# Kernel optimization log

Hardware: AMD Instinct MI355X
Metric: run time of the kernel (lower is better)

The kernel has to match this reference:

```python
import jax, jax.numpy as jnp
import numpy as np

NUM_USERS = 100000
NUM_ITEMS = 200000
EMB_DIM = 64
NUM_LAYERS = 3
NUM_INTER = 1000000
BATCH = 16384


def setup_inputs() -> dict:
    key = jax.random.key(0)
    k1, k2, k3, k4, k5, k6, k7 = jax.random.split(key, 7)
    # xavier-uniform-ish init for embeddings
    bound_u = float(np.sqrt(6.0 / (NUM_USERS + EMB_DIM)))
    bound_i = float(np.sqrt(6.0 / (NUM_ITEMS + EMB_DIM)))
    user_emb = jax.random.uniform(k1, (NUM_USERS, EMB_DIM), jnp.float32, -bound_u, bound_u)
    item_emb = jax.random.uniform(k2, (NUM_ITEMS, EMB_DIM), jnp.float32, -bound_i, bound_i)
    layer_weights = jax.random.uniform(k3, (NUM_LAYERS + 1,), jnp.float32)
    inter_users = jax.random.randint(k4, (NUM_INTER,), 0, NUM_USERS, jnp.int32)
    inter_items = jax.random.randint(k5, (NUM_INTER,), 0, NUM_ITEMS, jnp.int32)
    user_ids = jax.random.randint(k6, (BATCH,), 0, NUM_USERS, jnp.int32)
    item_ids = jax.random.randint(k7, (BATCH,), 0, NUM_ITEMS, jnp.int32)
    return {
        "user_emb": user_emb,
        "item_emb": item_emb,
        "layer_weights": layer_weights,
        "inter_users": inter_users,
        "inter_items": inter_items,
        "user_ids": user_ids,
        "item_ids": item_ids,
    }


def reference(user_emb, item_emb, layer_weights, inter_users, inter_items, user_ids, item_ids):
    n_users = user_emb.shape[0]
    n_items = item_emb.shape[0]
    n_nodes = n_users + n_items

    # Symmetrized bipartite edge list: (u -> i+n_users) and (i+n_users -> u)
    rows = inter_users
    cols = inter_items + n_users
    src = jnp.concatenate([rows, cols])  # [2E]
    dst = jnp.concatenate([cols, rows])  # [2E]

    # Symmetric degree normalization: D^{-1/2} A D^{-1/2}
    deg = jax.ops.segment_sum(jnp.ones_like(src, dtype=jnp.float32), src,
                              num_segments=n_nodes)
    dinv = jnp.where(deg > 0, jax.lax.rsqrt(jnp.maximum(deg, 1.0)) * (deg > 0), 0.0)
    dinv = jnp.where(deg > 0, deg ** -0.5, 0.0)
    edge_w = dinv[src] * dinv[dst]  # [2E]

    emb = jnp.concatenate([user_emb, item_emb], axis=0)  # [N, D]
    weights = jax.nn.softmax(layer_weights)

    final = weights[0] * emb
    for layer in range(NUM_LAYERS):
        # SpMM: out[src] += w * emb[dst]
        emb = jax.ops.segment_sum(edge_w[:, None] * emb[dst], src,
                                  num_segments=n_nodes)
        final = final + weights[layer + 1] * emb

    u_final = final[:n_users]
    i_final = final[n_users:]

    user_vectors = u_final[user_ids]   # [B, D]
    item_vectors = i_final[item_ids]   # [B, D]
    scores = jnp.sum(user_vectors * item_vectors, axis=1)  # [B]
    return scores
```

## Files before the change

### kernel.cpp

```cpp
#include <hip/hip_runtime.h>
#include <math.h>

#define NUM_USERS 100000
#define NUM_ITEMS 200000
#define N_NODES   300000
#define EMB       64
#define NUM_INTER 1000000
#define BATCH     16384

#define BSHIFT 9
#define BNODES 512
#define NBKT   ((N_NODES + BNODES - 1) / BNODES)
#define CAP    6144
#define RSHIFT 13
#define RSLOTS (1 << RSHIFT)
#define EDGES_PER_BLOCK 4096
#define AB_BLOCKS ((NUM_INTER + EDGES_PER_BLOCK - 1) / EDGES_PER_BLOCK)
#define QMARK_BLOCKS ((BATCH * 2) / 256)

#define PROP_BLOCKS ((N_NODES * 8 + 255) / 256)

typedef int      vint4 __attribute__((ext_vector_type(4)));
typedef _Float16 half8 __attribute__((ext_vector_type(8)));

#define PMASK 0x7FFFFu

__global__ __launch_bounds__(256) void bucket_scatter_k(
        const int* __restrict__ iu, const int* __restrict__ ii,
        const int* __restrict__ uid, const int* __restrict__ iid,
        int* __restrict__ cursor , unsigned* __restrict__ pairs,
        unsigned char* __restrict__ qflag, unsigned char* __restrict__ flag,
        const float* __restrict__ lw, float* __restrict__ w4,
        _Float16* __restrict__ semb, _Float16* __restrict__ z1, _Float16* __restrict__ z2) {
    int tid = threadIdx.x;
    if (blockIdx.x < QMARK_BLOCKS) {
        int t = blockIdx.x * 256 + tid;
        int node = (t & 1) ? (NUM_USERS + iid[t >> 1]) : uid[t >> 1];
        qflag[node] = 1;
        flag[node]  = 1;
        return;
    }
    if (blockIdx.x == QMARK_BLOCKS) {
        if (tid < 96) {
            unsigned* p = (tid < 32) ? (unsigned*)semb : (tid < 64) ? (unsigned*)z1 : (unsigned*)z2;
            p[(size_t)N_NODES * 32 + (tid & 31)] = 0u;
        }
        if (tid == 0) {
            float a = lw[0], b = lw[1], c = lw[2], d = lw[3];
            float m = fmaxf(fmaxf(a, b), fmaxf(c, d));
            float e0 = expf(a - m), e1 = expf(b - m), e2 = expf(c - m), e3 = expf(d - m);
            float sm = e0 + e1 + e2 + e3;
            w4[0] = e0 / sm; w4[1] = e1 / sm; w4[2] = e2 / sm; w4[3] = e3 / sm;
        }
        return;
    }
    __shared__ int hist[NBKT];
    __shared__ int gbase[NBKT];
    int bid = blockIdx.x - QMARK_BLOCKS - 1;
    for (int b = tid; b < NBKT; b += 256) hist[b] = 0;
    __syncthreads();

    int e0 = bid * EDGES_PER_BLOCK;
    int u[16], it[16];
    unsigned pk[32];
    #pragma unroll
    for (int k = 0; k < 16; ++k) {
        int e = e0 + k * 256 + tid;
        bool v = (e < NUM_INTER);
        u[k]  = v ? iu[e] : -1;
        it[k] = v ? (NUM_USERS + ii[e]) : -1;
    }
    #pragma unroll
    for (int k = 0; k < 16; ++k) {
        if (u[k] >= 0) {
            int b0 = u[k] >> BSHIFT;
            int r0 = atomicAdd(&hist[b0], 1);
            pk[2 * k] = ((unsigned)b0 << 13) | (unsigned)r0;
            int b1 = it[k] >> BSHIFT;
            int r1 = atomicAdd(&hist[b1], 1);
            pk[2 * k + 1] = ((unsigned)b1 << 13) | (unsigned)r1;
        }
    }
    __syncthreads();
    for (int b = tid; b < NBKT; b += 256) {
        int c = hist[b];
        if (c) gbase[b] = atomicAdd(&cursor[b * 16], c);
    }
    __syncthreads();
    #pragma unroll
    for (int k = 0; k < 16; ++k) {
        if (u[k] >= 0) {
            unsigned p0 = pk[2 * k];
            int b0 = (int)(p0 >> 13);
            int s0 = gbase[b0] + (int)(p0 & 0x1fffu);
            if (s0 < CAP)
                pairs[(size_t)b0 * CAP + s0] =
                    ((unsigned)(u[k] & (BNODES - 1)) << 19) | (unsigned)it[k];
            unsigned p1 = pk[2 * k + 1];
            int b1 = (int)(p1 >> 13);
            int s1 = gbase[b1] + (int)(p1 & 0x1fffu);
            if (s1 < CAP)
                pairs[(size_t)b1 * CAP + s1] =
                    ((unsigned)(it[k] & (BNODES - 1)) << 19) | (unsigned)u[k];
        }
    }
}

__global__ __launch_bounds__(256) void bucket_all_k(
        const int* __restrict__ cursor, const unsigned* __restrict__ pairs,
        const unsigned char* __restrict__ qflag, unsigned char* __restrict__ flag,
        int* __restrict__ deg, float* __restrict__ dinv, float* __restrict__ d2,
        float* __restrict__ rcp, int* __restrict__ row_start, int* __restrict__ nbr,
        const float* __restrict__ ue, const float* __restrict__ ie,
        _Float16* __restrict__ semb) {
    __shared__ int cnt[BNODES];
    __shared__ int lofs_s[BNODES];
    __shared__ float dinv_s[BNODES];
    __shared__ int sc[256];
    __shared__ unsigned qf[BNODES / 4];
    int b = blockIdx.x, tid = threadIdx.x;
    cnt[tid] = 0; cnt[tid + 256] = 0;
    if (tid < BNODES / 4)
        qf[tid] = ((const unsigned*)(qflag + ((size_t)b << BSHIFT)))[tid];
    __syncthreads();
    int n = cursor[b * 16]; if (n > CAP) n = CAP;
    const unsigned* p = pairs + (size_t)b * CAP;
    const unsigned char* qfb = (const unsigned char*)qf;
    for (int j = tid; j < n; j += 256) {
        unsigned code = p[j];
        int l = (int)(code >> 19);
        atomicAdd(&cnt[l], 1);
        if (qfb[l]) flag[code & PMASK] = 1;
    }
    __syncthreads();

    int l0 = 2 * tid, l1 = l0 + 1;
    int c0 = cnt[l0], c1 = cnt[l1];
    int p0 = (c0 + 3) & ~3, p1 = (c1 + 3) & ~3;
    int s = p0 + p1;
    sc[tid] = s;
    __syncthreads();
    for (int o = 1; o < 256; o <<= 1) {
        int x = (tid >= o) ? sc[tid - o] : 0;
        __syncthreads();
        sc[tid] += x;
        __syncthreads();
    }
    int excl = sc[tid] - s;
    int gb = b << BSHIFT;
    int g0 = gb + l0, g1 = gb + l1;
    float fd0 = (float)c0, fd1 = (float)c1;
    float di0 = (c0 > 0) ? (1.0f / sqrtf(fd0)) : 0.0f;
    float di1 = (c1 > 0) ? (1.0f / sqrtf(fd1)) : 0.0f;
    if (g0 < N_NODES) {
        deg[g0] = c0; dinv[g0] = di0;
        d2[g0]  = (c0 > 0) ? (1.0f / fd0) : 0.0f;
        rcp[g0] = (c0 > 0) ? sqrtf(fd0) : 0.0f;
        row_start[g0] = (b << RSHIFT) + excl;
    }
    if (g1 < N_NODES) {
        deg[g1] = c1; dinv[g1] = di1;
        d2[g1]  = (c1 > 0) ? (1.0f / fd1) : 0.0f;
        rcp[g1] = (c1 > 0) ? sqrtf(fd1) : 0.0f;
        row_start[g1] = (b << RSHIFT) + excl + p0;
    }
    lofs_s[l0] = excl; lofs_s[l1] = excl + p0;
    dinv_s[l0] = di0;  dinv_s[l1] = di1;
    cnt[l0] = 0; cnt[l1] = 0;
    __syncthreads();

    int nbase = b << RSHIFT;
    for (int j = tid; j < n; j += 256) {
        unsigned code = p[j];
        int l = (int)(code >> 19);
        int r = atomicAdd(&cnt[l], 1);
        nbr[nbase + lofs_s[l] + r] = (int)(code & PMASK);
    }
    for (int t = tid; t < BNODES * 8; t += 256) {
        int nl = t >> 3, q = t & 7;
        int node = gb + nl;
        if (node < N_NODES) {
            const float4* src = (node < NUM_USERS)
                ? (const float4*)ue + (size_t)node * 16
                : (const float4*)ie + (size_t)(node - NUM_USERS) * 16;
            float4 f0 = src[q * 2];
            float4 f1 = src[q * 2 + 1];
            float sdi = dinv_s[nl];
            half8 h;
            h[0] = (_Float16)(sdi * f0.x); h[1] = (_Float16)(sdi * f0.y);
            h[2] = (_Float16)(sdi * f0.z); h[3] = (_Float16)(sdi * f0.w);
            h[4] = (_Float16)(sdi * f1.x); h[5] = (_Float16)(sdi * f1.y);
            h[6] = (_Float16)(sdi * f1.z); h[7] = (_Float16)(sdi * f1.w);
            ((half8*)semb)[(size_t)node * 8 + q] = h;
        }
    }
}

__global__ void prop_first_k(const int* __restrict__ row_start, const int* __restrict__ nbr,
                             const int* __restrict__ deg, const float* __restrict__ d2,
                             const _Float16* __restrict__ semb, _Float16* __restrict__ z1) {
    int t = blockIdx.x * blockDim.x + threadIdx.x;
    int node = t >> 3;
    int q = t & 7;
    if (node >= N_NODES) return;
    int d = deg[node];
    int beg = row_start[node];
    int lim = beg + d;
    int end = beg + ((d + 3) & ~3);
    const half8* src = (const half8*)semb;
    float a0 = 0.f, a1 = 0.f, a2 = 0.f, a3 = 0.f, a4 = 0.f, a5 = 0.f, a6 = 0.f, a7 = 0.f;
    for (int j = beg; j < end; j += 8) {
        vint4 na = __builtin_nontemporal_load((const vint4*)(nbr + j));
        vint4 nb = __builtin_nontemporal_load((const vint4*)(nbr + j + 4));
        #pragma unroll
        for (int k = 0; k < 8; ++k) {
            int id = (j + k < lim) ? ((k < 4) ? na[k] : nb[k - 4]) : N_NODES;
            half8 h = src[(size_t)id * 8 + q];
            a0 += (float)h[0]; a1 += (float)h[1]; a2 += (float)h[2]; a3 += (float)h[3];
            a4 += (float)h[4]; a5 += (float)h[5]; a6 += (float)h[6]; a7 += (float)h[7];
        }
    }
    float s = d2[node];
    half8 r;
    r[0] = (_Float16)(s * a0); r[1] = (_Float16)(s * a1);
    r[2] = (_Float16)(s * a2); r[3] = (_Float16)(s * a3);
    r[4] = (_Float16)(s * a4); r[5] = (_Float16)(s * a5);
    r[6] = (_Float16)(s * a6); r[7] = (_Float16)(s * a7);
    ((half8*)z1)[(size_t)node * 8 + q] = r;
}

__global__ void prop_masked_k(const int* __restrict__ row_start, const int* __restrict__ nbr,
                              const int* __restrict__ deg, const float* __restrict__ d2,
                              const unsigned char* __restrict__ flag,
                              const _Float16* __restrict__ in, _Float16* __restrict__ out) {
    int t = blockIdx.x * blockDim.x + threadIdx.x;
    int node = t >> 3;
    int q = t & 7;
    if (node >= N_NODES) return;
    if (!flag[node]) return;
    int d = deg[node];
    int beg = row_start[node];
    int lim = beg + d;
    int end = beg + ((d + 3) & ~3);
    const half8* src = (const half8*)in;
    float a0 = 0.f, a1 = 0.f, a2 = 0.f, a3 = 0.f, a4 = 0.f, a5 = 0.f, a6 = 0.f, a7 = 0.f;
    for (int j = beg; j < end; j += 8) {
        vint4 na = __builtin_nontemporal_load((const vint4*)(nbr + j));
        vint4 nb = __builtin_nontemporal_load((const vint4*)(nbr + j + 4));
        #pragma unroll
        for (int k = 0; k < 8; ++k) {
            int id = (j + k < lim) ? ((k < 4) ? na[k] : nb[k - 4]) : N_NODES;
            half8 h = src[(size_t)id * 8 + q];
            a0 += (float)h[0]; a1 += (float)h[1]; a2 += (float)h[2]; a3 += (float)h[3];
            a4 += (float)h[4]; a5 += (float)h[5]; a6 += (float)h[6]; a7 += (float)h[7];
        }
    }
    float s = d2[node];
    half8 r;
    r[0] = (_Float16)(s * a0); r[1] = (_Float16)(s * a1);
    r[2] = (_Float16)(s * a2); r[3] = (_Float16)(s * a3);
    r[4] = (_Float16)(s * a4); r[5] = (_Float16)(s * a5);
    r[6] = (_Float16)(s * a6); r[7] = (_Float16)(s * a7);
    ((half8*)out)[(size_t)node * 8 + q] = r;
}

__global__ void fused_score_k(const int* __restrict__ row_start, const int* __restrict__ nbr,
                              const int* __restrict__ deg,
                              const float* __restrict__ dinv, const float* __restrict__ rcp,
                              const float* __restrict__ ue, const float* __restrict__ ie,
                              const _Float16* __restrict__ z1, const _Float16* __restrict__ z2,
                              const int* __restrict__ uid, const int* __restrict__ iid,
                              const float* __restrict__ w4, float* __restrict__ out) {
    int t = blockIdx.x * blockDim.x + threadIdx.x;
    int slot = t >> 4;
    if (slot >= BATCH) return;
    int within = t & 15;
    int side = within >> 3;
    int q = within & 7;

    int node;
    const float4* erow;
    if (side == 0) {
        int u = uid[slot];
        node = u;
        erow = (const float4*)ue + (size_t)u * 16;
    } else {
        int ii_ = iid[slot];
        node = NUM_USERS + ii_;
        erow = (const float4*)ie + (size_t)ii_ * 16;
    }

    float w0 = w4[0], w1 = w4[1], w2 = w4[2], w3 = w4[3];
    int d = deg[node];
    int beg = row_start[node];
    int lim = beg + d;
    int end = beg + ((d + 3) & ~3);
    const half8* z2v = (const half8*)z2;

    float a0 = 0.f, a1 = 0.f, a2 = 0.f, a3 = 0.f, a4 = 0.f, a5 = 0.f, a6 = 0.f, a7 = 0.f;
    for (int j = beg; j < end; j += 8) {
        vint4 na = __builtin_nontemporal_load((const vint4*)(nbr + j));
        vint4 nb = __builtin_nontemporal_load((const vint4*)(nbr + j + 4));
        #pragma unroll
        for (int k = 0; k < 8; ++k) {
            int id = (j + k < lim) ? ((k < 4) ? na[k] : nb[k - 4]) : N_NODES;
            half8 h = z2v[(size_t)id * 8 + q];
            a0 += (float)h[0]; a1 += (float)h[1]; a2 += (float)h[2]; a3 += (float)h[3];
            a4 += (float)h[4]; a5 += (float)h[5]; a6 += (float)h[6]; a7 += (float)h[7];
        }
    }

    float r  = rcp[node];
    float di = dinv[node];
    float e[8];
    *reinterpret_cast<float4*>(&e[0]) = erow[q * 2];
    *reinterpret_cast<float4*>(&e[4]) = erow[q * 2 + 1];
    half8 h1 = ((const half8*)z1)[(size_t)node * 8 + q];
    half8 h2 = z2v[(size_t)node * 8 + q];
    float acc[8] = {a0, a1, a2, a3, a4, a5, a6, a7};

    float f[8];
    #pragma unroll
    for (int dd = 0; dd < 8; ++dd)
        f[dd] = w0 * e[dd] + r * (w1 * (float)h1[dd] + w2 * (float)h2[dd]) + w3 * di * acc[dd];

    float pr = 0.f;
    #pragma unroll
    for (int dd = 0; dd < 8; ++dd) {
        float o = __shfl_xor(f[dd], 8);
        pr += f[dd] * o;
    }
    pr += __shfl_xor(pr, 1);
    pr += __shfl_xor(pr, 2);
    pr += __shfl_xor(pr, 4);

    if (within == 0) out[slot] = pr;
}


extern "C" void kernel_launch(void* const* d_in, const int* in_sizes, int n_in,
                              void* d_out, int out_size, void* d_ws, size_t ws_size,
                              hipStream_t stream) {
    const float* user_emb = (const float*)d_in[0];
    const float* item_emb = (const float*)d_in[1];
    const float* layer_w  = (const float*)d_in[2];
    const int*   inter_u  = (const int*)d_in[3];
    const int*   inter_i  = (const int*)d_in[4];
    const int*   user_ids = (const int*)d_in[5];
    const int*   item_ids = (const int*)d_in[6];
    float* out = (float*)d_out;

    char* base = (char*)d_ws;
    size_t off = 0;
    auto alloc = [&](size_t bytes) -> char* {
        char* p = base + off;
        off = (off + bytes + 255) & ~(size_t)255;
        return p;
    };
    float*    w4        = (float*)    alloc(4 * sizeof(float));
    int*      deg       = (int*)      alloc((size_t)N_NODES * sizeof(int));
    float*    dinv      = (float*)    alloc((size_t)N_NODES * sizeof(float));
    float*    d2        = (float*)    alloc((size_t)N_NODES * sizeof(float));
    float*    rcp       = (float*)    alloc((size_t)N_NODES * sizeof(float));
    int*      row_start = (int*)      alloc((size_t)N_NODES * sizeof(int));
    unsigned char* flag   = (unsigned char*)alloc((size_t)N_NODES + 256);
    unsigned char* qflag  = (unsigned char*)alloc((size_t)N_NODES + 512);
    int*           cursor = (int*)          alloc((size_t)NBKT * 16 * sizeof(int));
    unsigned* pairs     = (unsigned*) alloc((size_t)NBKT * CAP * sizeof(unsigned));
    int*      csr_nbr   = (int*)      alloc((size_t)NBKT * RSLOTS * sizeof(int));
    _Float16* semb      = (_Float16*) alloc(((size_t)N_NODES + 1) * EMB * sizeof(_Float16));
    _Float16* zA        = (_Float16*) alloc(((size_t)N_NODES + 1) * EMB * sizeof(_Float16));
    _Float16* zB        = (_Float16*) alloc(((size_t)N_NODES + 1) * EMB * sizeof(_Float16));

    size_t span = (size_t)((char*)cursor - (char*)flag) + (size_t)NBKT * 16 * sizeof(int);
    hipMemsetAsync(flag, 0, span, stream);

    bucket_scatter_k<<<QMARK_BLOCKS + 1 + AB_BLOCKS, 256, 0, stream>>>(
        inter_u, inter_i, user_ids, item_ids, cursor, pairs, qflag, flag,
        layer_w, w4, semb, zB, zA);

    bucket_all_k<<<NBKT, 256, 0, stream>>>(
        cursor, pairs, qflag, flag, deg, dinv, d2, rcp, row_start, csr_nbr,
        user_emb, item_emb, semb);

    prop_first_k<<<PROP_BLOCKS, 256, 0, stream>>>(
        row_start, csr_nbr, deg, d2, semb, zB);

    prop_masked_k<<<PROP_BLOCKS, 256, 0, stream>>>(
        row_start, csr_nbr, deg, d2, flag, zB, zA);

    fused_score_k<<<(BATCH * 16 + 255) / 256, 256, 0, stream>>>(
        row_start, csr_nbr, deg, dinv, rcp, user_emb, item_emb,
        zB , zA , user_ids, item_ids, w4, out);
}
```

Baseline: 267.5 us.

## Move fp32-to-fp16 embedding conversion into scatter kernel, apply dinv per neighbor

The fp32 to fp16 conversion of the embedding table moves out of the CSR-build kernel and into extra blocks of the earlier scatter kernel, so it no longer waits on degree computation. Because dinv is not known at that point, the stored fp16 embeddings are left unscaled. Instead, prop_first_k loads dinv[id] for each neighbor and multiplies it in during accumulation. This shortens the serial bucket_all_k stage, at the cost of one extra scattered 4-byte load per edge in the first propagation and an extra sentinel dinv entry.

```diff
diff --git a/kernel.cpp b/kernel.cpp
--- a/kernel.cpp
+++ b/kernel.cpp
@@ -17,6 +17,8 @@
 #define EDGES_PER_BLOCK 4096
 #define AB_BLOCKS ((NUM_INTER + EDGES_PER_BLOCK - 1) / EDGES_PER_BLOCK)
 #define QMARK_BLOCKS ((BATCH * 2) / 256)
+#define CONV_BLOCKS ((N_NODES * 8 + 255) / 256)
+#define CONV_BASE   (QMARK_BLOCKS + 1 + AB_BLOCKS)
 
 #define PROP_BLOCKS ((N_NODES * 8 + 255) / 256)
 
@@ -31,6 +33,8 @@
         int* __restrict__ cursor , unsigned* __restrict__ pairs,
         unsigned char* __restrict__ qflag, unsigned char* __restrict__ flag,
         const float* __restrict__ lw, float* __restrict__ w4,
+        float* __restrict__ dinv,
+        const float* __restrict__ ue, const float* __restrict__ ie,
         _Float16* __restrict__ semb, _Float16* __restrict__ z1, _Float16* __restrict__ z2) {
     int tid = threadIdx.x;
     if (blockIdx.x < QMARK_BLOCKS) {
@@ -45,6 +49,7 @@
             unsigned* p = (tid < 32) ? (unsigned*)semb : (tid < 64) ? (unsigned*)z1 : (unsigned*)z2;
             p[(size_t)N_NODES * 32 + (tid & 31)] = 0u;
         }
+        if (tid == 96) dinv[N_NODES] = 0.0f;
         if (tid == 0) {
             float a = lw[0], b = lw[1], c = lw[2], d = lw[3];
             float m = fmaxf(fmaxf(a, b), fmaxf(c, d));
@@ -52,6 +57,24 @@
             float sm = e0 + e1 + e2 + e3;
             w4[0] = e0 / sm; w4[1] = e1 / sm; w4[2] = e2 / sm; w4[3] = e3 / sm;
         }
+        return;
+    }
+    if (blockIdx.x >= CONV_BASE) {
+        int t = (blockIdx.x - CONV_BASE) * 256 + tid;
+        int node = t >> 3;
+        int q = t & 7;
+        if (node >= N_NODES) return;
+        const float4* src = (node < NUM_USERS)
+            ? (const float4*)ue + (size_t)node * 16
+            : (const float4*)ie + (size_t)(node - NUM_USERS) * 16;
+        float4 f0 = src[q * 2];
+        float4 f1 = src[q * 2 + 1];
+        half8 h;
+        h[0] = (_Float16)f0.x; h[1] = (_Float16)f0.y;
+        h[2] = (_Float16)f0.z; h[3] = (_Float16)f0.w;
+        h[4] = (_Float16)f1.x; h[5] = (_Float16)f1.y;
+        h[6] = (_Float16)f1.z; h[7] = (_Float16)f1.w;
+        ((half8*)semb)[(size_t)node * 8 + q] = h;
         return;
     }
     __shared__ int hist[NBKT];
@@ -110,12 +133,9 @@
         const int* __restrict__ cursor, const unsigned* __restrict__ pairs,
         const unsigned char* __restrict__ qflag, unsigned char* __restrict__ flag,
         int* __restrict__ deg, float* __restrict__ dinv, float* __restrict__ d2,
-        float* __restrict__ rcp, int* __restrict__ row_start, int* __restrict__ nbr,
-        const float* __restrict__ ue, const float* __restrict__ ie,
-        _Float16* __restrict__ semb) {
+        float* __restrict__ rcp, int* __restrict__ row_start, int* __restrict__ nbr) {
     __shared__ int cnt[BNODES];
     __shared__ int lofs_s[BNODES];
-    __shared__ float dinv_s[BNODES];
     __shared__ int sc[256];
     __shared__ unsigned qf[BNODES / 4];
     int b = blockIdx.x, tid = threadIdx.x;
@@ -150,22 +170,21 @@
     int gb = b << BSHIFT;
     int g0 = gb + l0, g1 = gb + l1;
     float fd0 = (float)c0, fd1 = (float)c1;
-    float di0 = (c0 > 0) ? (1.0f / sqrtf(fd0)) : 0.0f;
-    float di1 = (c1 > 0) ? (1.0f / sqrtf(fd1)) : 0.0f;
     if (g0 < N_NODES) {
-        deg[g0] = c0; dinv[g0] = di0;
+        deg[g0] = c0;
+        dinv[g0] = (c0 > 0) ? (1.0f / sqrtf(fd0)) : 0.0f;
         d2[g0]  = (c0 > 0) ? (1.0f / fd0) : 0.0f;
         rcp[g0] = (c0 > 0) ? sqrtf(fd0) : 0.0f;
         row_start[g0] = (b << RSHIFT) + excl;
     }
     if (g1 < N_NODES) {
-        deg[g1] = c1; dinv[g1] = di1;
+        deg[g1] = c1;
+        dinv[g1] = (c1 > 0) ? (1.0f / sqrtf(fd1)) : 0.0f;
         d2[g1]  = (c1 > 0) ? (1.0f / fd1) : 0.0f;
         rcp[g1] = (c1 > 0) ? sqrtf(fd1) : 0.0f;
         row_start[g1] = (b << RSHIFT) + excl + p0;
     }
     lofs_s[l0] = excl; lofs_s[l1] = excl + p0;
-    dinv_s[l0] = di0;  dinv_s[l1] = di1;
     cnt[l0] = 0; cnt[l1] = 0;
     __syncthreads();
 
@@ -176,28 +195,11 @@
         int r = atomicAdd(&cnt[l], 1);
         nbr[nbase + lofs_s[l] + r] = (int)(code & PMASK);
     }
-    for (int t = tid; t < BNODES * 8; t += 256) {
-        int nl = t >> 3, q = t & 7;
-        int node = gb + nl;
-        if (node < N_NODES) {
-            const float4* src = (node < NUM_USERS)
-                ? (const float4*)ue + (size_t)node * 16
-                : (const float4*)ie + (size_t)(node - NUM_USERS) * 16;
-            float4 f0 = src[q * 2];
-            float4 f1 = src[q * 2 + 1];
-            float sdi = dinv_s[nl];
-            half8 h;
-            h[0] = (_Float16)(sdi * f0.x); h[1] = (_Float16)(sdi * f0.y);
-            h[2] = (_Float16)(sdi * f0.z); h[3] = (_Float16)(sdi * f0.w);
-            h[4] = (_Float16)(sdi * f1.x); h[5] = (_Float16)(sdi * f1.y);
-            h[6] = (_Float16)(sdi * f1.z); h[7] = (_Float16)(sdi * f1.w);
-            ((half8*)semb)[(size_t)node * 8 + q] = h;
-        }
-    }
 }
 
 __global__ void prop_first_k(const int* __restrict__ row_start, const int* __restrict__ nbr,
                              const int* __restrict__ deg, const float* __restrict__ d2,
+                             const float* __restrict__ dinv,
                              const _Float16* __restrict__ semb, _Float16* __restrict__ z1) {
     int t = blockIdx.x * blockDim.x + threadIdx.x;
     int node = t >> 3;
@@ -215,9 +217,12 @@
         #pragma unroll
         for (int k = 0; k < 8; ++k) {
             int id = (j + k < lim) ? ((k < 4) ? na[k] : nb[k - 4]) : N_NODES;
+            float w = dinv[id];
             half8 h = src[(size_t)id * 8 + q];
-            a0 += (float)h[0]; a1 += (float)h[1]; a2 += (float)h[2]; a3 += (float)h[3];
-            a4 += (float)h[4]; a5 += (float)h[5]; a6 += (float)h[6]; a7 += (float)h[7];
+            a0 += w * (float)h[0]; a1 += w * (float)h[1];
+            a2 += w * (float)h[2]; a3 += w * (float)h[3];
+            a4 += w * (float)h[4]; a5 += w * (float)h[5];
+            a6 += w * (float)h[6]; a7 += w * (float)h[7];
         }
     }
     float s = d2[node];
@@ -359,7 +364,7 @@
     };
     float*    w4        = (float*)    alloc(4 * sizeof(float));
     int*      deg       = (int*)      alloc((size_t)N_NODES * sizeof(int));
-    float*    dinv      = (float*)    alloc((size_t)N_NODES * sizeof(float));
+    float*    dinv      = (float*)    alloc(((size_t)N_NODES + 1) * sizeof(float));
     float*    d2        = (float*)    alloc((size_t)N_NODES * sizeof(float));
     float*    rcp       = (float*)    alloc((size_t)N_NODES * sizeof(float));
     int*      row_start = (int*)      alloc((size_t)N_NODES * sizeof(int));
@@ -375,16 +380,15 @@
     size_t span = (size_t)((char*)cursor - (char*)flag) + (size_t)NBKT * 16 * sizeof(int);
     hipMemsetAsync(flag, 0, span, stream);
 
-    bucket_scatter_k<<<QMARK_BLOCKS + 1 + AB_BLOCKS, 256, 0, stream>>>(
+    bucket_scatter_k<<<QMARK_BLOCKS + 1 + AB_BLOCKS + CONV_BLOCKS, 256, 0, stream>>>(
         inter_u, inter_i, user_ids, item_ids, cursor, pairs, qflag, flag,
-        layer_w, w4, semb, zB, zA);
+        layer_w, w4, dinv, user_emb, item_emb, semb, zB, zA);
 
     bucket_all_k<<<NBKT, 256, 0, stream>>>(
-        cursor, pairs, qflag, flag, deg, dinv, d2, rcp, row_start, csr_nbr,
-        user_emb, item_emb, semb);
+        cursor, pairs, qflag, flag, deg, dinv, d2, rcp, row_start, csr_nbr);
 
     prop_first_k<<<PROP_BLOCKS, 256, 0, stream>>>(
-        row_start, csr_nbr, deg, d2, semb, zB);
+        row_start, csr_nbr, deg, d2, dinv, semb, zB);
 
     prop_masked_k<<<PROP_BLOCKS, 256, 0, stream>>>(
         row_start, csr_nbr, deg, d2, flag, zB, zA);
```

Result: faster. 260.0 us (-2.8%).
